# Kernel optimization log

Measured on AMD Instinct MI355X. Metric: run time of the kernel, lower is better.

## Reference

```python
import jax, jax.numpy as jnp
import numpy as np

N = 100000      # nodes
E = 1600000     # directed edges (before self-loops)
IN = 128        # in_channels
HID = 64        # hidden_channels
LH = 4          # local heads
GH = 2          # global heads
NC = 2          # num_classes
BN_EPS = 1e-5
NEG_SLOPE = 0.2


def setup_inputs() -> dict:
    key = jax.random.key(0)
    ks = jax.random.split(key, 24)
    def nrm(k, shape, fan_in):
        return jax.random.normal(k, shape, dtype=jnp.float32) / np.sqrt(fan_in)
    inp = {
        "x": jax.random.normal(ks[0], (N, IN), dtype=jnp.float32),
        "edge_index": jax.random.randint(ks[1], (2, E), 0, N, dtype=jnp.int64),
        # local GATConv: IN -> HID, heads=LH, concat
        "w1": nrm(ks[2], (IN, LH * HID), IN),
        "a_src1": nrm(ks[3], (LH, HID), HID),
        "a_dst1": nrm(ks[4], (LH, HID), HID),
        "b1": jnp.zeros((LH * HID,), jnp.float32),
        # BN1 over LH*HID
        "g1": jnp.ones((LH * HID,), jnp.float32),
        "be1": jnp.zeros((LH * HID,), jnp.float32),
        "m1": 0.1 * jax.random.normal(ks[5], (LH * HID,), dtype=jnp.float32),
        "v1": 0.5 + jax.random.uniform(ks[6], (LH * HID,), dtype=jnp.float32),
        # global GATConv: LH*HID -> HID, heads=GH, concat=False (mean)
        "w2": nrm(ks[7], (LH * HID, GH * HID), LH * HID),
        "a_src2": nrm(ks[8], (GH, HID), HID),
        "a_dst2": nrm(ks[9], (GH, HID), HID),
        "b2": jnp.zeros((HID,), jnp.float32),
        # BN2 over HID
        "g2": jnp.ones((HID,), jnp.float32),
        "be2": jnp.zeros((HID,), jnp.float32),
        "m2": 0.1 * jax.random.normal(ks[10], (HID,), dtype=jnp.float32),
        "v2": 0.5 + jax.random.uniform(ks[11], (HID,), dtype=jnp.float32),
        # classifier HID -> NC
        "wc": nrm(ks[12], (HID, NC), HID),
        "bc": jnp.zeros((NC,), jnp.float32),
    }
    return inp


def _gat_conv(x, src, dst, W, att_src, att_dst, bias, heads, out_c, concat):
    n = x.shape[0]
    h = (x @ W).reshape(n, heads, out_c)           # [N,H,C]
    a_s = jnp.sum(h * att_src, axis=-1)            # [N,H]
    a_d = jnp.sum(h * att_dst, axis=-1)            # [N,H]
    e = jax.nn.leaky_relu(a_s[src] + a_d[dst], NEG_SLOPE)  # [E,H]
    # segment softmax over destination node
    mx = jax.ops.segment_max(e, dst, num_segments=n)
    e = jnp.exp(e - mx[dst])
    den = jax.ops.segment_sum(e, dst, num_segments=n)
    alpha = e / (den[dst] + 1e-16)                 # [E,H]
    msg = h[src] * alpha[:, :, None]               # [E,H,C]
    out = jax.ops.segment_sum(msg, dst, num_segments=n)   # [N,H,C]
    out = out.reshape(n, heads * out_c) if concat else out.mean(axis=1)
    return out + bias


def _bn_eval(x, gamma, beta, mean, var):
    return (x - mean) * (gamma / jnp.sqrt(var + BN_EPS)) + beta


def reference(x, edge_index, w1, a_src1, a_dst1, b1, g1, be1, m1, v1,
              w2, a_src2, a_dst2, b2, g2, be2, m2, v2, wc, bc):
    n = x.shape[0]
    loops = jnp.arange(n, dtype=edge_index.dtype)
    src = jnp.concatenate([edge_index[0], loops])  # PyG adds self-loops
    dst = jnp.concatenate([edge_index[1], loops])
    # local attention layer
    h = _gat_conv(x, src, dst, w1, a_src1, a_dst1, b1, LH, HID, True)
    h = jax.nn.elu(_bn_eval(h, g1, be1, m1, v1))
    # global attention layer (last: mean over heads, no activation)
    h = _gat_conv(h, src, dst, w2, a_src2, a_dst2, b2, GH, HID, False)
    h = _bn_eval(h, g2, be2, m2, v2)
    return h @ wc + bc                             # [N, NC] logits
```

## Files before the change

kernel.cpp:

```cpp
#include <hip/hip_runtime.h>
#include <hip/hip_fp16.h>
#include <math.h>

#define NN 100000
#define EE 1600000
#define ETOT (EE + NN)
#define BN_EPS 1e-5f
#define NEG_SLOPE 0.2f
#define NBLK ((NN + 255) / 256)
#define NGRP 8
#define GRPSZ ((NN + NGRP - 1) / NGRP)
#define HISTBLK 2048

typedef _Float16 half8 __attribute__((ext_vector_type(8)));
typedef float f32x4 __attribute__((ext_vector_type(4)));

__device__ __forceinline__ float lrelu(float x) { return fmaxf(x, NEG_SLOPE * x); }
__device__ __forceinline__ float wsum(float v) {
#pragma unroll
    for (int m = 32; m; m >>= 1) v += __shfl_xor(v, m, 64);
    return v;
}
__device__ __forceinline__ float gsum16(float v) {
#pragma unroll
    for (int m = 1; m < 16; m <<= 1) v += __shfl_xor(v, m, 64);
    return v;
}
__device__ __forceinline__ unsigned packh2(float a, float b) {
    __half2 p = __float22half2_rn(make_float2(a, b));
    return *reinterpret_cast<unsigned*>(&p);
}

__global__ __launch_bounds__(256) void k_preph(
    const float* __restrict__ b1, const float* __restrict__ g1,
    const float* __restrict__ be1, const float* __restrict__ m1,
    const float* __restrict__ v1,
    const float* __restrict__ b2, const float* __restrict__ g2,
    const float* __restrict__ be2, const float* __restrict__ m2,
    const float* __restrict__ v2, const float* __restrict__ wc,
    const float* __restrict__ bc,
    const float* __restrict__ w1, const float* __restrict__ w2,
    const float* __restrict__ as1w, const float* __restrict__ ad1w,
    const int* __restrict__ ei,
    float* __restrict__ scs, float* __restrict__ shs,
    float* __restrict__ wq, float* __restrict__ cst,
    float* __restrict__ va, float* __restrict__ vd,
    _Float16* __restrict__ wt1, _Float16* __restrict__ wt2,
    int* __restrict__ counts)
{
    const int b = blockIdx.x, t = threadIdx.x;
    if (b == 0) {
        const float sc = g1[t] * rsqrtf(v1[t] + BN_EPS);
        scs[t] = sc;
        shs[t] = (b1[t] - m1[t]) * sc + be1[t];
    } else if (b == 1) {
        if (t < 64) {
            const float s2 = g2[t] * rsqrtf(v2[t] + BN_EPS);
            wq[t * 2 + 0] = s2 * wc[t * 2 + 0];
            wq[t * 2 + 1] = s2 * wc[t * 2 + 1];
            const float tv = (b2[t] - m2[t]) * s2 + be2[t];
            const float c0 = wsum(tv * wc[t * 2 + 0]);
            const float c1 = wsum(tv * wc[t * 2 + 1]);
            if (t == 0) { cst[0] = c0 + bc[0]; cst[1] = c1 + bc[1]; }
        }
    } else if (b < 130) {
        const int idx = (b - 2) * 256 + t;
        const int n = idx >> 7, k = idx & 127;
        wt1[idx] = (_Float16)w1[k * 256 + n];
    } else if (b < 258) {
        const int idx = (b - 130) * 256 + t;
        const int n = idx >> 8, k = idx & 255;
        wt2[idx] = (_Float16)w2[k * 128 + n];
    } else if (b == 258) {
#pragma unroll
        for (int rep = 0; rep < 2; ++rep) {
            const int idx = rep * 256 + t;
            const int h = idx >> 7, k = idx & 127;
            float sa = 0.f, sd = 0.f;
            for (int c = 0; c < 64; ++c) {
                const float wv = w1[k * 256 + h * 64 + c];
                sa = fmaf(wv, as1w[h * 64 + c], sa);
                sd = fmaf(wv, ad1w[h * 64 + c], sd);
            }
            va[idx] = sa;
            vd[idx] = sd;
        }
    } else {
        const int bh = b - 259;
        const int g = bh & (NGRP - 1);
        const int lo = g * GRPSZ;
        const int hi = (lo + GRPSZ < NN) ? lo + GRPSZ : NN;
        const int stride = (HISTBLK >> 3) * 256;
        for (int e = (bh >> 3) * 256 + t; e < EE; e += stride) {
            const int d = ei[EE + e];
            if (d >= lo && d < hi) atomicAdd(&counts[d], 1);
        }
    }
}

__global__ __launch_bounds__(256) void k_scan_bsum(const int* __restrict__ counts,
                                                   int* __restrict__ bsum) {
    __shared__ int sd[256];
    const int i = blockIdx.x * 256 + threadIdx.x;
    sd[threadIdx.x] = (i < NN) ? counts[i] + 1 : 0;
    __syncthreads();
    for (int s2 = 128; s2; s2 >>= 1) {
        if (threadIdx.x < s2) sd[threadIdx.x] += sd[threadIdx.x + s2];
        __syncthreads();
    }
    if (threadIdx.x == 0) bsum[blockIdx.x] = sd[0];
}
__global__ __launch_bounds__(256) void k_scan_finaltop(
    const int* __restrict__ counts, const int* __restrict__ bsum,
    int* __restrict__ rowptr, int* __restrict__ srcs, int* __restrict__ cursor)
{
    __shared__ int sd[256];
    int partial = 0;
    for (int j = threadIdx.x; j < NBLK; j += 256)
        if (j < blockIdx.x) partial += bsum[j];
    sd[threadIdx.x] = partial;
    __syncthreads();
    for (int s2 = 128; s2; s2 >>= 1) {
        if (threadIdx.x < s2) sd[threadIdx.x] += sd[threadIdx.x + s2];
        __syncthreads();
    }
    const int base = sd[0];
    __syncthreads();
    const int i = blockIdx.x * 256 + threadIdx.x;
    const int orig = (i < NN) ? counts[i] + 1 : 0;
    sd[threadIdx.x] = orig;
    __syncthreads();
    for (int off = 1; off < 256; off <<= 1) {
        const int v = (threadIdx.x >= off) ? sd[threadIdx.x - off] : 0;
        __syncthreads();
        sd[threadIdx.x] += v;
        __syncthreads();
    }
    if (i < NN) {
        const int rp = base + sd[threadIdx.x] - orig;
        rowptr[i] = rp;
        srcs[rp] = i;
        cursor[i] = rp + 1;
        if (i == NN - 1) rowptr[NN] = ETOT;
    }
}
__global__ __launch_bounds__(256) void k_scatter8(const int* __restrict__ ei,
                                                  int* __restrict__ srcs,
                                                  int* __restrict__ cursor) {
    const int g = blockIdx.x & (NGRP - 1);
    const int lo = g * GRPSZ;
    const int hi = (lo + GRPSZ < NN) ? lo + GRPSZ : NN;
    const int nb = gridDim.x >> 3;
    const int stride = nb * 256;
    for (int e = (blockIdx.x >> 3) * 256 + threadIdx.x; e < EE; e += stride) {
        const int d = ei[EE + e];
        if (d >= lo && d < hi) {
            const int p = atomicAdd(&cursor[d], 1);
            srcs[p] = ei[e];
        }
    }
}

__global__ __launch_bounds__(256) void k_xcvt(
    const float* __restrict__ x, const float* __restrict__ va,
    const float* __restrict__ vd, _Float16* __restrict__ xh,
    float* __restrict__ as_, float* __restrict__ ad_)
{
    const int gid = blockIdx.x * 256 + threadIdx.x;
    const int n = gid >> 4;
    if (n >= NN) return;
    const int j = gid & 15;
    const int k0 = j * 8;
    float xv[8];
    *(float4*)&xv[0] = *(const float4*)&x[(size_t)n * 128 + k0];
    *(float4*)&xv[4] = *(const float4*)&x[(size_t)n * 128 + k0 + 4];
    half8 hv;
#pragma unroll
    for (int i = 0; i < 8; ++i) hv[i] = (_Float16)xv[i];
    *(half8*)&xh[(size_t)n * 128 + k0] = hv;
    float sa[4], sd[4];
#pragma unroll
    for (int h = 0; h < 4; ++h) {
        float s = 0.f, d = 0.f;
#pragma unroll
        for (int i = 0; i < 8; ++i) {
            s = fmaf(xv[i], va[h * 128 + k0 + i], s);
            d = fmaf(xv[i], vd[h * 128 + k0 + i], d);
        }
        sa[h] = gsum16(s);
        sd[h] = gsum16(d);
    }
    if (j == 0) {
        *(float4*)&as_[n * 4] = make_float4(sa[0], sa[1], sa[2], sa[3]);
        *(float4*)&ad_[n * 4] = make_float4(sd[0], sd[1], sd[2], sd[3]);
    }
}

__global__ __launch_bounds__(256) void k_agg1x(
    const int* __restrict__ rowptr, const int* __restrict__ srcs,
    const _Float16* __restrict__ xh, const float* __restrict__ as_,
    const float* __restrict__ ad_, _Float16* __restrict__ y)
{
    const int d = blockIdx.x * 4 + (threadIdx.x >> 6);
    if (d >= NN) return;
    const int lane = threadIdx.x & 63;
    const int r0 = rowptr[d], r1 = rowptr[d + 1];
    const int h = lane >> 4;
    const int cb = (lane & 15) * 8;
    const float myad = ad_[d * 4 + h];

    float den = 0.f;
    float acc[8] = {0.f, 0.f, 0.f, 0.f, 0.f, 0.f, 0.f, 0.f};
    int k = r0;
    for (; k + 3 < r1; k += 4) {
        const int sm = srcs[k + (lane & 3)];
        const float pm = __expf(lrelu(as_[sm * 4 + h] + myad));
        const int s0 = __shfl(sm, 0, 64);
        const int s1 = __shfl(sm, 1, 64);
        const int s2 = __shfl(sm, 2, 64);
        const int s3 = __shfl(sm, 3, 64);
        const int pb = lane & 48;
        const float p0 = __shfl(pm, pb | 0, 64);
        const float p1 = __shfl(pm, pb | 1, 64);
        const float p2 = __shfl(pm, pb | 2, 64);
        const float p3 = __shfl(pm, pb | 3, 64);
        den += (p0 + p1) + (p2 + p3);
        const half8 v0 = *(const half8*)&xh[(size_t)s0 * 128 + cb];
        const half8 v1 = *(const half8*)&xh[(size_t)s1 * 128 + cb];
        const half8 v2 = *(const half8*)&xh[(size_t)s2 * 128 + cb];
        const half8 v3 = *(const half8*)&xh[(size_t)s3 * 128 + cb];
#pragma unroll
        for (int i = 0; i < 8; ++i) {
            acc[i] = fmaf(p0, (float)v0[i], acc[i]);
            acc[i] = fmaf(p1, (float)v1[i], acc[i]);
            acc[i] = fmaf(p2, (float)v2[i], acc[i]);
            acc[i] = fmaf(p3, (float)v3[i], acc[i]);
        }
    }
    for (; k < r1; ++k) {
        const int s = srcs[k];
        const float p = __expf(lrelu(as_[s * 4 + h] + myad));
        den += p;
        const half8 v = *(const half8*)&xh[(size_t)s * 128 + cb];
#pragma unroll
        for (int i = 0; i < 8; ++i) acc[i] = fmaf(p, (float)v[i], acc[i]);
    }
    const float inv = 1.f / (den + 1e-16f);
    half8 hv;
#pragma unroll
    for (int i = 0; i < 8; ++i) hv[i] = (_Float16)(acc[i] * inv);
    *(half8*)&y[(size_t)d * 512 + h * 128 + cb] = hv;
}

__global__ __launch_bounds__(256) void k_l2fuse(
    const _Float16* __restrict__ y,
    const _Float16* __restrict__ wt1,
    const _Float16* __restrict__ wt2,
    const float* __restrict__ scs, const float* __restrict__ shs,
    const float* __restrict__ asrc, const float* __restrict__ adst,
    const float* __restrict__ wq,
    float* __restrict__ ad_, uint2* __restrict__ pack)
{
    __shared__ _Float16 ys[64][136];
    __shared__ _Float16 mid[64][264];
    const int n0 = blockIdx.x * 64;
    const int t = threadIdx.x;
    const int l = t & 63, w = t >> 6;
    const int lc = l & 15, kq = (l >> 4) * 8, lr = (l >> 4) * 4;
    const int m0w = (w & 1) * 32;
    const f32x4 fzero = {0.f, 0.f, 0.f, 0.f};

    const int c0w = (w >> 1) * 32;
    for (int h = 0; h < 4; ++h) {
        if (h) __syncthreads();
#pragma unroll
        for (int i = 0; i < 4; ++i) {
            const int f = i * 2048 + t * 8;
            const int m = f >> 7, k8 = f & 127;
            half8 v = {};
            if (n0 + m < NN)
                v = *(const half8*)&y[(size_t)(n0 + m) * 512 + h * 128 + k8];
            *(half8*)&ys[m][k8] = v;
        }
        __syncthreads();

        f32x4 acc[2][2];
        acc[0][0] = fzero; acc[0][1] = fzero; acc[1][0] = fzero; acc[1][1] = fzero;
#pragma unroll
        for (int ks = 0; ks < 4; ++ks) {
            const int k0 = ks * 32 + kq;
            const half8 a0 = *(const half8*)&ys[m0w + lc][k0];
            const half8 a1 = *(const half8*)&ys[m0w + 16 + lc][k0];
            const half8 b0 = *(const half8*)&wt1[(size_t)(h * 64 + c0w + lc) * 128 + k0];
            const half8 b1 = *(const half8*)&wt1[(size_t)(h * 64 + c0w + 16 + lc) * 128 + k0];
            acc[0][0] = __builtin_amdgcn_mfma_f32_16x16x32_f16(a0, b0, acc[0][0], 0, 0, 0);
            acc[0][1] = __builtin_amdgcn_mfma_f32_16x16x32_f16(a0, b1, acc[0][1], 0, 0, 0);
            acc[1][0] = __builtin_amdgcn_mfma_f32_16x16x32_f16(a1, b0, acc[1][0], 0, 0, 0);
            acc[1][1] = __builtin_amdgcn_mfma_f32_16x16x32_f16(a1, b1, acc[1][1], 0, 0, 0);
        }
#pragma unroll
        for (int c = 0; c < 2; ++c) {
            const int col = h * 64 + c0w + c * 16 + lc;
            const float scv = scs[col], shv = shs[col];
#pragma unroll
            for (int r = 0; r < 2; ++r) {
#pragma unroll
                for (int i = 0; i < 4; ++i) {
                    float e = fmaf(acc[r][c][i], scv, shv);
                    e = e > 0.f ? e : __expf(e) - 1.f;
                    mid[m0w + r * 16 + lr + i][col] = (_Float16)e;
                }
            }
        }
    }
    __syncthreads();

    const int c20 = (w >> 1) * 64;
    f32x4 acc2[2][4];
#pragma unroll
    for (int r = 0; r < 2; ++r)
#pragma unroll
        for (int c = 0; c < 4; ++c) acc2[r][c] = fzero;
#pragma unroll
    for (int ks = 0; ks < 8; ++ks) {
        const int k0 = ks * 32 + kq;
        const half8 a0 = *(const half8*)&mid[m0w + lc][k0];
        const half8 a1 = *(const half8*)&mid[m0w + 16 + lc][k0];
#pragma unroll
        for (int c = 0; c < 4; ++c) {
            const half8 b = *(const half8*)&wt2[(size_t)(c20 + c * 16 + lc) * 256 + k0];
            acc2[0][c] = __builtin_amdgcn_mfma_f32_16x16x32_f16(a0, b, acc2[0][c], 0, 0, 0);
            acc2[1][c] = __builtin_amdgcn_mfma_f32_16x16x32_f16(a1, b, acc2[1][c], 0, 0, 0);
        }
    }
    const int head = w >> 1;
    float awv[4], dwv[4], wq0[4], wq1[4];
#pragma unroll
    for (int c = 0; c < 4; ++c) {
        const int j = c20 + c * 16 + lc;
        const int cl = j & 63;
        awv[c] = asrc[j];
        dwv[c] = adst[j];
        wq0[c] = wq[cl * 2 + 0];
        wq1[c] = wq[cl * 2 + 1];
    }
#pragma unroll
    for (int r = 0; r < 2; ++r) {
#pragma unroll
        for (int i = 0; i < 4; ++i) {
            float s = 0.f, d = 0.f, q0 = 0.f, q1 = 0.f;
#pragma unroll
            for (int c = 0; c < 4; ++c) {
                s = fmaf(acc2[r][c][i], awv[c], s);
                d = fmaf(acc2[r][c][i], dwv[c], d);
                q0 = fmaf(acc2[r][c][i], wq0[c], q0);
                q1 = fmaf(acc2[r][c][i], wq1[c], q1);
            }
            s = gsum16(s); d = gsum16(d); q0 = gsum16(q0); q1 = gsum16(q1);
            const int rg = n0 + m0w + r * 16 + lr + i;
            if (lc == 0 && rg < NN) {
                ad_[rg * 2 + head] = d;
                uint2 u;
                u.x = __float_as_uint(s);
                u.y = packh2(q0, q1);
                pack[rg * 2 + head] = u;
            }
        }
    }
}

__global__ __launch_bounds__(256) void k_agg2q(
    const int* __restrict__ rowptr, const int* __restrict__ srcs,
    const uint4* __restrict__ pack, const float* __restrict__ ad_,
    const float* __restrict__ cst, float* __restrict__ out)
{
    const int d = blockIdx.x * 16 + (threadIdx.x >> 4);
    if (d >= NN) return;
    const int il = threadIdx.x & 15;
    const int r0 = rowptr[d], r1 = rowptr[d + 1];
    const float2 adv = *(const float2*)&ad_[d * 2];

    float den0 = 0.f, den1 = 0.f;
    float qa00 = 0.f, qa01 = 0.f, qa10 = 0.f, qa11 = 0.f;
    for (int k = r0 + il; k < r1; k += 16) {
        const int s = srcs[k];
        const uint4 rec = pack[s];
        const float a0 = __uint_as_float(rec.x);
        const float a1 = __uint_as_float(rec.z);
        const float2 q0 = __half22float2(*reinterpret_cast<const __half2*>(&rec.y));
        const float2 q1 = __half22float2(*reinterpret_cast<const __half2*>(&rec.w));
        const float p0 = __expf(lrelu(a0 + adv.x));
        const float p1 = __expf(lrelu(a1 + adv.y));
        den0 += p0; den1 += p1;
        qa00 = fmaf(p0, q0.x, qa00); qa01 = fmaf(p0, q0.y, qa01);
        qa10 = fmaf(p1, q1.x, qa10); qa11 = fmaf(p1, q1.y, qa11);
    }
    den0 = gsum16(den0); den1 = gsum16(den1);
    qa00 = gsum16(qa00); qa01 = gsum16(qa01);
    qa10 = gsum16(qa10); qa11 = gsum16(qa11);
    if (il == 0) {
        const float i0 = 1.f / (den0 + 1e-16f);
        const float i1 = 1.f / (den1 + 1e-16f);
        out[d * 2 + 0] = cst[0] + 0.5f * (qa00 * i0 + qa10 * i1);
        out[d * 2 + 1] = cst[1] + 0.5f * (qa01 * i0 + qa11 * i1);
    }
}

extern "C" void kernel_launch(void* const* d_in, const int* in_sizes, int n_in,
                              void* d_out, int out_size, void* d_ws, size_t ws_size,
                              hipStream_t stream) {
    const float* x      = (const float*)d_in[0];
    const int*   ei     = (const int*)d_in[1];
    const float* w1     = (const float*)d_in[2];
    const float* a_src1 = (const float*)d_in[3];
    const float* a_dst1 = (const float*)d_in[4];
    const float* b1     = (const float*)d_in[5];
    const float* g1     = (const float*)d_in[6];
    const float* be1    = (const float*)d_in[7];
    const float* m1     = (const float*)d_in[8];
    const float* v1     = (const float*)d_in[9];
    const float* w2     = (const float*)d_in[10];
    const float* a_src2 = (const float*)d_in[11];
    const float* a_dst2 = (const float*)d_in[12];
    const float* b2     = (const float*)d_in[13];
    const float* g2     = (const float*)d_in[14];
    const float* be2    = (const float*)d_in[15];
    const float* m2     = (const float*)d_in[16];
    const float* v2     = (const float*)d_in[17];
    const float* wc     = (const float*)d_in[18];
    const float* bc     = (const float*)d_in[19];
    float* out = (float*)d_out;

    float* ws = (float*)d_ws;
    _Float16* xh = (_Float16*)ws;
    _Float16* y  = (_Float16*)(ws + (size_t)NN * 64);
    float* C = ws + (size_t)NN * 320;

    float* as1 = C;
    float* ad1 = C + (size_t)NN * 4;
    float* ad2 = C + (size_t)NN * 8;
    float* packf = C + (size_t)NN * 10;
    float* scs = C + (size_t)NN * 14;
    float* shs = scs + 256;
    float* wq  = shs + 256;
    float* cst = wq + 128;
    float* va  = cst + 64;
    float* vd  = va + 512;
    float* wbase = vd + 512;
    _Float16* wt1 = (_Float16*)wbase;
    _Float16* wt2 = wt1 + 32768;
    int* counts = (int*)(wbase + 32768);
    int* rowptr = counts + NN;
    int* bsum   = rowptr + NN + 63;
    int* srcs   = bsum + 512;

    hipMemsetAsync(counts, 0, (size_t)NN * sizeof(int), stream);
    k_preph<<<259 + HISTBLK, 256, 0, stream>>>(
        b1, g1, be1, m1, v1, b2, g2, be2, m2, v2, wc, bc, w1, w2,
        a_src1, a_dst1, ei, scs, shs, wq, cst, va, vd, wt1, wt2, counts);

    k_scan_bsum<<<NBLK, 256, 0, stream>>>(counts, bsum);
    k_scan_finaltop<<<NBLK, 256, 0, stream>>>(counts, bsum, rowptr, srcs, counts);
    k_scatter8<<<2048, 256, 0, stream>>>(ei, srcs, counts);

    k_xcvt<<<(NN * 16 + 255) / 256, 256, 0, stream>>>(x, va, vd, xh, as1, ad1);
    k_agg1x<<<(NN + 3) / 4, 256, 0, stream>>>(rowptr, srcs, xh, as1, ad1, y);

    k_l2fuse<<<(NN + 63) / 64, 256, 0, stream>>>(y, wt1, wt2, scs, shs,
                                                 a_src2, a_dst2, wq,
                                                 ad2, (uint2*)packf);

    k_agg2q<<<(NN + 15) / 16, 256, 0, stream>>>(rowptr, srcs, (const uint4*)packf,
                                                ad2, cst, out);
}
```

Before: 360.2 us.

## Fuse layer-1 aggregation with projection and fold W2 into precomputed vectors

Merges the layer-1 neighbour aggregation and the layer-1 projection/BN/ELU into one kernel, so the per-node aggregate stays in shared memory instead of making a round trip through a 100k×512 fp16 buffer in global memory. It also folds W2 algebraically into eight 256-long vectors (attention src/dst and the classifier projection per head), which replaces the second MFMA GEMM with dot products. The cost is fewer blocks carrying more work each: every wave now aggregates four nodes serially. Precision also changes, since the layer-2 quantities are now computed from fp32 ELU outputs against fp32 folded vectors.

```diff
diff --git a/kernel.cpp b/kernel.cpp
--- a/kernel.cpp
+++ b/kernel.cpp
@@ -41,11 +41,13 @@
     const float* __restrict__ bc,
     const float* __restrict__ w1, const float* __restrict__ w2,
     const float* __restrict__ as1w, const float* __restrict__ ad1w,
+    const float* __restrict__ as2w, const float* __restrict__ ad2w,
     const int* __restrict__ ei,
     float* __restrict__ scs, float* __restrict__ shs,
-    float* __restrict__ wq, float* __restrict__ cst,
+    float* __restrict__ cst,
     float* __restrict__ va, float* __restrict__ vd,
-    _Float16* __restrict__ wt1, _Float16* __restrict__ wt2,
+    float* __restrict__ uvec,
+    _Float16* __restrict__ wt1,
     int* __restrict__ counts)
 {
     const int b = blockIdx.x, t = threadIdx.x;
@@ -56,8 +58,6 @@
     } else if (b == 1) {
         if (t < 64) {
             const float s2 = g2[t] * rsqrtf(v2[t] + BN_EPS);
-            wq[t * 2 + 0] = s2 * wc[t * 2 + 0];
-            wq[t * 2 + 1] = s2 * wc[t * 2 + 1];
             const float tv = (b2[t] - m2[t]) * s2 + be2[t];
             const float c0 = wsum(tv * wc[t * 2 + 0]);
             const float c1 = wsum(tv * wc[t * 2 + 1]);
@@ -67,11 +67,7 @@
         const int idx = (b - 2) * 256 + t;
         const int n = idx >> 7, k = idx & 127;
         wt1[idx] = (_Float16)w1[k * 256 + n];
-    } else if (b < 258) {
-        const int idx = (b - 130) * 256 + t;
-        const int n = idx >> 8, k = idx & 255;
-        wt2[idx] = (_Float16)w2[k * 128 + n];
-    } else if (b == 258) {
+    } else if (b == 130) {
 #pragma unroll
         for (int rep = 0; rep < 2; ++rep) {
             const int idx = rep * 256 + t;
@@ -85,8 +81,28 @@
             va[idx] = sa;
             vd[idx] = sd;
         }
+    } else if (b == 131) {
+        const int k = t;
+        float s[8] = {0.f, 0.f, 0.f, 0.f, 0.f, 0.f, 0.f, 0.f};
+        for (int c = 0; c < 64; ++c) {
+            const float s2c = g2[c] * rsqrtf(v2[c] + BN_EPS);
+            const float wq0 = s2c * wc[c * 2 + 0];
+            const float wq1 = s2c * wc[c * 2 + 1];
+            const float w20 = w2[k * 128 + c];
+            const float w21 = w2[k * 128 + 64 + c];
+            s[0] = fmaf(w20, as2w[c], s[0]);
+            s[1] = fmaf(w21, as2w[64 + c], s[1]);
+            s[2] = fmaf(w20, ad2w[c], s[2]);
+            s[3] = fmaf(w21, ad2w[64 + c], s[3]);
+            s[4] = fmaf(w20, wq0, s[4]);
+            s[5] = fmaf(w20, wq1, s[5]);
+            s[6] = fmaf(w21, wq0, s[6]);
+            s[7] = fmaf(w21, wq1, s[7]);
+        }
+#pragma unroll
+        for (int u = 0; u < 8; ++u) uvec[u * 256 + k] = s[u];
     } else {
-        const int bh = b - 259;
+        const int bh = b - 132;
         const int g = bh & (NGRP - 1);
         const int lo = g * GRPSZ;
         const int hi = (lo + GRPSZ < NN) ? lo + GRPSZ : NN;
@@ -196,176 +212,140 @@
     }
 }
 
-__global__ __launch_bounds__(256) void k_agg1x(
+__global__ __launch_bounds__(256) void k_fused1(
     const int* __restrict__ rowptr, const int* __restrict__ srcs,
     const _Float16* __restrict__ xh, const float* __restrict__ as_,
-    const float* __restrict__ ad_, _Float16* __restrict__ y)
+    const float* __restrict__ ad_,
+    const _Float16* __restrict__ wt1,
+    const float* __restrict__ scs, const float* __restrict__ shs,
+    const float* __restrict__ uvec,
+    float* __restrict__ ad2, uint2* __restrict__ pack)
 {
-    const int d = blockIdx.x * 4 + (threadIdx.x >> 6);
-    if (d >= NN) return;
-    const int lane = threadIdx.x & 63;
-    const int r0 = rowptr[d], r1 = rowptr[d + 1];
-    const int h = lane >> 4;
-    const int cb = (lane & 15) * 8;
-    const float myad = ad_[d * 4 + h];
-
-    float den = 0.f;
-    float acc[8] = {0.f, 0.f, 0.f, 0.f, 0.f, 0.f, 0.f, 0.f};
-    int k = r0;
-    for (; k + 3 < r1; k += 4) {
-        const int sm = srcs[k + (lane & 3)];
-        const float pm = __expf(lrelu(as_[sm * 4 + h] + myad));
-        const int s0 = __shfl(sm, 0, 64);
-        const int s1 = __shfl(sm, 1, 64);
-        const int s2 = __shfl(sm, 2, 64);
-        const int s3 = __shfl(sm, 3, 64);
-        const int pb = lane & 48;
-        const float p0 = __shfl(pm, pb | 0, 64);
-        const float p1 = __shfl(pm, pb | 1, 64);
-        const float p2 = __shfl(pm, pb | 2, 64);
-        const float p3 = __shfl(pm, pb | 3, 64);
-        den += (p0 + p1) + (p2 + p3);
-        const half8 v0 = *(const half8*)&xh[(size_t)s0 * 128 + cb];
-        const half8 v1 = *(const half8*)&xh[(size_t)s1 * 128 + cb];
-        const half8 v2 = *(const half8*)&xh[(size_t)s2 * 128 + cb];
-        const half8 v3 = *(const half8*)&xh[(size_t)s3 * 128 + cb];
-#pragma unroll
-        for (int i = 0; i < 8; ++i) {
-            acc[i] = fmaf(p0, (float)v0[i], acc[i]);
-            acc[i] = fmaf(p1, (float)v1[i], acc[i]);
-            acc[i] = fmaf(p2, (float)v2[i], acc[i]);
-            acc[i] = fmaf(p3, (float)v3[i], acc[i]);
-        }
-    }
-    for (; k < r1; ++k) {
-        const int s = srcs[k];
-        const float p = __expf(lrelu(as_[s * 4 + h] + myad));
-        den += p;
-        const half8 v = *(const half8*)&xh[(size_t)s * 128 + cb];
-#pragma unroll
-        for (int i = 0; i < 8; ++i) acc[i] = fmaf(p, (float)v[i], acc[i]);
-    }
-    const float inv = 1.f / (den + 1e-16f);
-    half8 hv;
-#pragma unroll
-    for (int i = 0; i < 8; ++i) hv[i] = (_Float16)(acc[i] * inv);
-    *(half8*)&y[(size_t)d * 512 + h * 128 + cb] = hv;
-}
-
-__global__ __launch_bounds__(256) void k_l2fuse(
-    const _Float16* __restrict__ y,
-    const _Float16* __restrict__ wt1,
-    const _Float16* __restrict__ wt2,
-    const float* __restrict__ scs, const float* __restrict__ shs,
-    const float* __restrict__ asrc, const float* __restrict__ adst,
-    const float* __restrict__ wq,
-    float* __restrict__ ad_, uint2* __restrict__ pack)
-{
-    __shared__ _Float16 ys[64][136];
-    __shared__ _Float16 mid[64][264];
-    const int n0 = blockIdx.x * 64;
+    __shared__ _Float16 ys[4][16][136];
+    __shared__ float red[4][8][16];
+    const int n0 = blockIdx.x * 16;
     const int t = threadIdx.x;
     const int l = t & 63, w = t >> 6;
-    const int lc = l & 15, kq = (l >> 4) * 8, lr = (l >> 4) * 4;
-    const int m0w = (w & 1) * 32;
+    const int h = l >> 4;
+    const int cb = (l & 15) * 8;
+
+    for (int nd = 0; nd < 4; ++nd) {
+        const int d = n0 + w * 4 + nd;
+        const int r0 = rowptr[d], r1 = rowptr[d + 1];
+        const float myad = ad_[d * 4 + h];
+        float den = 0.f;
+        float acc[8] = {0.f, 0.f, 0.f, 0.f, 0.f, 0.f, 0.f, 0.f};
+        int k = r0;
+        for (; k + 3 < r1; k += 4) {
+            const int sm = srcs[k + (l & 3)];
+            const float pm = __expf(lrelu(as_[sm * 4 + h] + myad));
+            const int s0 = __shfl(sm, 0, 64);
+            const int s1 = __shfl(sm, 1, 64);
+            const int s2 = __shfl(sm, 2, 64);
+            const int s3 = __shfl(sm, 3, 64);
+            const int pb = l & 48;
+            const float p0 = __shfl(pm, pb | 0, 64);
+            const float p1 = __shfl(pm, pb | 1, 64);
+            const float p2 = __shfl(pm, pb | 2, 64);
+            const float p3 = __shfl(pm, pb | 3, 64);
+            den += (p0 + p1) + (p2 + p3);
+            const half8 v0 = *(const half8*)&xh[(size_t)s0 * 128 + cb];
+            const half8 v1 = *(const half8*)&xh[(size_t)s1 * 128 + cb];
+            const half8 v2 = *(const half8*)&xh[(size_t)s2 * 128 + cb];
+            const half8 v3 = *(const half8*)&xh[(size_t)s3 * 128 + cb];
+#pragma unroll
+            for (int i = 0; i < 8; ++i) {
+                acc[i] = fmaf(p0, (float)v0[i], acc[i]);
+                acc[i] = fmaf(p1, (float)v1[i], acc[i]);
+                acc[i] = fmaf(p2, (float)v2[i], acc[i]);
+                acc[i] = fmaf(p3, (float)v3[i], acc[i]);
+            }
+        }
+        for (; k < r1; ++k) {
+            const int s = srcs[k];
+            const float p = __expf(lrelu(as_[s * 4 + h] + myad));
+            den += p;
+            const half8 v = *(const half8*)&xh[(size_t)s * 128 + cb];
+#pragma unroll
+            for (int i = 0; i < 8; ++i) acc[i] = fmaf(p, (float)v[i], acc[i]);
+        }
+        const float inv = 1.f / (den + 1e-16f);
+        half8 hv;
+#pragma unroll
+        for (int i = 0; i < 8; ++i) hv[i] = (_Float16)(acc[i] * inv);
+        *(half8*)&ys[h][w * 4 + nd][cb] = hv;
+    }
+    __syncthreads();
+
+    const int lc = l & 15, kq = (l >> 4) * 8;
     const f32x4 fzero = {0.f, 0.f, 0.f, 0.f};
-
-    const int c0w = (w >> 1) * 32;
-    for (int h = 0; h < 4; ++h) {
-        if (h) __syncthreads();
+    f32x4 pacc[4];
+#pragma unroll
+    for (int c = 0; c < 4; ++c) pacc[c] = fzero;
+#pragma unroll
+    for (int ks = 0; ks < 4; ++ks) {
+        const int k0 = ks * 32 + kq;
+        const half8 a = *(const half8*)&ys[w][lc][k0];
+#pragma unroll
+        for (int c = 0; c < 4; ++c) {
+            const half8 b = *(const half8*)&wt1[(size_t)(w * 64 + c * 16 + lc) * 128 + k0];
+            pacc[c] = __builtin_amdgcn_mfma_f32_16x16x32_f16(a, b, pacc[c], 0, 0, 0);
+        }
+    }
+
+    float uv[8][4], scv[4], shv[4];
+#pragma unroll
+    for (int c = 0; c < 4; ++c) {
+        const int cg = w * 64 + c * 16 + lc;
+        scv[c] = scs[cg];
+        shv[c] = shs[cg];
+#pragma unroll
+        for (int u = 0; u < 8; ++u) uv[u][c] = uvec[u * 256 + cg];
+    }
+    float e[4][4];
+#pragma unroll
+    for (int c = 0; c < 4; ++c)
 #pragma unroll
         for (int i = 0; i < 4; ++i) {
-            const int f = i * 2048 + t * 8;
-            const int m = f >> 7, k8 = f & 127;
-            half8 v = {};
-            if (n0 + m < NN)
-                v = *(const half8*)&y[(size_t)(n0 + m) * 512 + h * 128 + k8];
-            *(half8*)&ys[m][k8] = v;
-        }
-        __syncthreads();
-
-        f32x4 acc[2][2];
-        acc[0][0] = fzero; acc[0][1] = fzero; acc[1][0] = fzero; acc[1][1] = fzero;
-#pragma unroll
-        for (int ks = 0; ks < 4; ++ks) {
-            const int k0 = ks * 32 + kq;
-            const half8 a0 = *(const half8*)&ys[m0w + lc][k0];
-            const half8 a1 = *(const half8*)&ys[m0w + 16 + lc][k0];
-            const half8 b0 = *(const half8*)&wt1[(size_t)(h * 64 + c0w + lc) * 128 + k0];
-            const half8 b1 = *(const half8*)&wt1[(size_t)(h * 64 + c0w + 16 + lc) * 128 + k0];
-            acc[0][0] = __builtin_amdgcn_mfma_f32_16x16x32_f16(a0, b0, acc[0][0], 0, 0, 0);
-            acc[0][1] = __builtin_amdgcn_mfma_f32_16x16x32_f16(a0, b1, acc[0][1], 0, 0, 0);
-            acc[1][0] = __builtin_amdgcn_mfma_f32_16x16x32_f16(a1, b0, acc[1][0], 0, 0, 0);
-            acc[1][1] = __builtin_amdgcn_mfma_f32_16x16x32_f16(a1, b1, acc[1][1], 0, 0, 0);
-        }
-#pragma unroll
-        for (int c = 0; c < 2; ++c) {
-            const int col = h * 64 + c0w + c * 16 + lc;
-            const float scv = scs[col], shv = shs[col];
-#pragma unroll
-            for (int r = 0; r < 2; ++r) {
-#pragma unroll
-                for (int i = 0; i < 4; ++i) {
-                    float e = fmaf(acc[r][c][i], scv, shv);
-                    e = e > 0.f ? e : __expf(e) - 1.f;
-                    mid[m0w + r * 16 + lr + i][col] = (_Float16)e;
-                }
-            }
-        }
-    }
-    __syncthreads();
-
-    const int c20 = (w >> 1) * 64;
-    f32x4 acc2[2][4];
-#pragma unroll
-    for (int r = 0; r < 2; ++r)
-#pragma unroll
-        for (int c = 0; c < 4; ++c) acc2[r][c] = fzero;
-#pragma unroll
-    for (int ks = 0; ks < 8; ++ks) {
-        const int k0 = ks * 32 + kq;
-        const half8 a0 = *(const half8*)&mid[m0w + lc][k0];
-        const half8 a1 = *(const half8*)&mid[m0w + 16 + lc][k0];
-#pragma unroll
-        for (int c = 0; c < 4; ++c) {
-            const half8 b = *(const half8*)&wt2[(size_t)(c20 + c * 16 + lc) * 256 + k0];
-            acc2[0][c] = __builtin_amdgcn_mfma_f32_16x16x32_f16(a0, b, acc2[0][c], 0, 0, 0);
-            acc2[1][c] = __builtin_amdgcn_mfma_f32_16x16x32_f16(a1, b, acc2[1][c], 0, 0, 0);
-        }
-    }
-    const int head = w >> 1;
-    float awv[4], dwv[4], wq0[4], wq1[4];
-#pragma unroll
-    for (int c = 0; c < 4; ++c) {
-        const int j = c20 + c * 16 + lc;
-        const int cl = j & 63;
-        awv[c] = asrc[j];
-        dwv[c] = adst[j];
-        wq0[c] = wq[cl * 2 + 0];
-        wq1[c] = wq[cl * 2 + 1];
-    }
-#pragma unroll
-    for (int r = 0; r < 2; ++r) {
+            float ev = fmaf(pacc[c][i], scv[c], shv[c]);
+            e[c][i] = ev > 0.f ? ev : __expf(ev) - 1.f;
+        }
+    float pu[8][4];
+#pragma unroll
+    for (int u = 0; u < 8; ++u)
 #pragma unroll
         for (int i = 0; i < 4; ++i) {
-            float s = 0.f, d = 0.f, q0 = 0.f, q1 = 0.f;
-#pragma unroll
-            for (int c = 0; c < 4; ++c) {
-                s = fmaf(acc2[r][c][i], awv[c], s);
-                d = fmaf(acc2[r][c][i], dwv[c], d);
-                q0 = fmaf(acc2[r][c][i], wq0[c], q0);
-                q1 = fmaf(acc2[r][c][i], wq1[c], q1);
-            }
-            s = gsum16(s); d = gsum16(d); q0 = gsum16(q0); q1 = gsum16(q1);
-            const int rg = n0 + m0w + r * 16 + lr + i;
-            if (lc == 0 && rg < NN) {
-                ad_[rg * 2 + head] = d;
-                uint2 u;
-                u.x = __float_as_uint(s);
-                u.y = packh2(q0, q1);
-                pack[rg * 2 + head] = u;
-            }
-        }
+            float s = 0.f;
+#pragma unroll
+            for (int c = 0; c < 4; ++c) s = fmaf(e[c][i], uv[u][c], s);
+            pu[u][i] = gsum16(s);
+        }
+    if (lc == 0) {
+        const int rbase = (l >> 4) * 4;
+#pragma unroll
+        for (int u = 0; u < 8; ++u)
+#pragma unroll
+            for (int i = 0; i < 4; ++i)
+                red[w][u][rbase + i] = pu[u][i];
+    }
+    __syncthreads();
+
+    if (t < 32) {
+        const int row = t >> 1, hh = t & 1;
+        const int rg = n0 + row;
+        float as = 0.f, dd = 0.f, q0 = 0.f, q1 = 0.f;
+#pragma unroll
+        for (int ww = 0; ww < 4; ++ww) {
+            as += red[ww][0 + hh][row];
+            dd += red[ww][2 + hh][row];
+            q0 += red[ww][4 + 2 * hh][row];
+            q1 += red[ww][5 + 2 * hh][row];
+        }
+        ad2[rg * 2 + hh] = dd;
+        uint2 u;
+        u.x = __float_as_uint(as);
+        u.y = packh2(q0, q1);
+        pack[rg * 2 + hh] = u;
     }
 }
 
@@ -433,8 +413,7 @@
 
     float* ws = (float*)d_ws;
     _Float16* xh = (_Float16*)ws;
-    _Float16* y  = (_Float16*)(ws + (size_t)NN * 64);
-    float* C = ws + (size_t)NN * 320;
+    float* C = ws + (size_t)NN * 64;
 
     float* as1 = C;
     float* ad1 = C + (size_t)NN * 4;
@@ -442,33 +421,32 @@
     float* packf = C + (size_t)NN * 10;
     float* scs = C + (size_t)NN * 14;
     float* shs = scs + 256;
-    float* wq  = shs + 256;
-    float* cst = wq + 128;
+    float* cst = shs + 256;
     float* va  = cst + 64;
     float* vd  = va + 512;
-    float* wbase = vd + 512;
+    float* uvec = vd + 512;
+    float* wbase = uvec + 2048;
     _Float16* wt1 = (_Float16*)wbase;
-    _Float16* wt2 = wt1 + 32768;
-    int* counts = (int*)(wbase + 32768);
+    int* counts = (int*)(wbase + 16384);
     int* rowptr = counts + NN;
     int* bsum   = rowptr + NN + 63;
     int* srcs   = bsum + 512;
 
     hipMemsetAsync(counts, 0, (size_t)NN * sizeof(int), stream);
-    k_preph<<<259 + HISTBLK, 256, 0, stream>>>(
+    k_preph<<<132 + HISTBLK, 256, 0, stream>>>(
         b1, g1, be1, m1, v1, b2, g2, be2, m2, v2, wc, bc, w1, w2,
-        a_src1, a_dst1, ei, scs, shs, wq, cst, va, vd, wt1, wt2, counts);
+        a_src1, a_dst1, a_src2, a_dst2, ei,
+        scs, shs, cst, va, vd, uvec, wt1, counts);
 
     k_scan_bsum<<<NBLK, 256, 0, stream>>>(counts, bsum);
     k_scan_finaltop<<<NBLK, 256, 0, stream>>>(counts, bsum, rowptr, srcs, counts);
     k_scatter8<<<2048, 256, 0, stream>>>(ei, srcs, counts);
 
     k_xcvt<<<(NN * 16 + 255) / 256, 256, 0, stream>>>(x, va, vd, xh, as1, ad1);
-    k_agg1x<<<(NN + 3) / 4, 256, 0, stream>>>(rowptr, srcs, xh, as1, ad1, y);
-
-    k_l2fuse<<<(NN + 63) / 64, 256, 0, stream>>>(y, wt1, wt2, scs, shs,
-                                                 a_src2, a_dst2, wq,
-                                                 ad2, (uint2*)packf);
+
+    k_fused1<<<NN / 16, 256, 0, stream>>>(rowptr, srcs, xh, as1, ad1,
+                                          wt1, scs, shs, uvec,
+                                          ad2, (uint2*)packf);
 
     k_agg2q<<<(NN + 15) / 16, 256, 0, stream>>>(rowptr, srcs, (const uint4*)packf,
                                                 ad2, cst, out);
```

Result: slower. 390.7 us (+8.5%).
